# Performance work log

Measured on AMD Instinct MI355X. Metric: run time of the kernel, lower is better.

Reference implementation:

```python
import jax, jax.numpy as jnp
import numpy as np

B, T, TQ, E = 32, 200, 50, 64
P, C = 128, 64
BN_EPS = 1e-6
DICE_EPS = 1e-6


def _bn(x, g, b, m, v):
    # inference-mode batch norm over last axis
    return (x - m) * jax.lax.rsqrt(v + BN_EPS) * g + b


def _dice(x, alpha, m, v):
    # Dice activation: p = sigmoid(BN(x, no scale/shift)); out = p*x + alpha*(1-p)*x
    p = jax.nn.sigmoid((x - m) * jax.lax.rsqrt(v + DICE_EPS))
    return p * x + alpha * (1.0 - p) * x


def setup_inputs() -> dict:
    key = jax.random.key(0)
    ks = jax.random.split(key, 16)
    def g(k, shape, scale=0.05):
        return jax.random.normal(k, shape, dtype=jnp.float32) * scale
    inp = {
        "user_behavior": jax.random.normal(ks[0], (B, T, E), dtype=jnp.float32),
        "items": jax.random.normal(ks[1], (B, TQ, E), dtype=jnp.float32),
        "user_profile": jax.random.normal(ks[2], (B, P), dtype=jnp.float32),
        "context": jax.random.normal(ks[3], (B, C), dtype=jnp.float32),
        # attention MLP
        "W1": g(ks[4], (4 * E, 36)), "b1": jnp.zeros((36,), jnp.float32),
        "dice_alpha": jnp.zeros((36,), jnp.float32),
        "dice_mean": jnp.zeros((36,), jnp.float32),
        "dice_var": jnp.ones((36,), jnp.float32),
        "W2": g(ks[5], (36, 1)), "b2": jnp.zeros((1,), jnp.float32),
        # trunk MLP (input dim E+P+C = 256)
        "bn1_g": jnp.ones((E + P + C,), jnp.float32), "bn1_b": jnp.zeros((E + P + C,), jnp.float32),
        "bn1_m": jnp.zeros((E + P + C,), jnp.float32), "bn1_v": jnp.ones((E + P + C,), jnp.float32),
        "Wm1": g(ks[6], (E + P + C, 256)), "bm1": jnp.zeros((256,), jnp.float32),
        "bn2_g": jnp.ones((256,), jnp.float32), "bn2_b": jnp.zeros((256,), jnp.float32),
        "bn2_m": jnp.zeros((256,), jnp.float32), "bn2_v": jnp.ones((256,), jnp.float32),
        "Wm2": g(ks[7], (256, 128)), "bm2": jnp.zeros((128,), jnp.float32),
        "bn3_g": jnp.ones((128,), jnp.float32), "bn3_b": jnp.zeros((128,), jnp.float32),
        "bn3_m": jnp.zeros((128,), jnp.float32), "bn3_v": jnp.ones((128,), jnp.float32),
        "Wm3": g(ks[8], (128, 64)), "bm3": jnp.zeros((64,), jnp.float32),
    }
    return inp


def reference(user_behavior, items, user_profile, context,
              W1, b1, dice_alpha, dice_mean, dice_var, W2, b2,
              bn1_g, bn1_b, bn1_m, bn1_v, Wm1, bm1,
              bn2_g, bn2_b, bn2_m, bn2_v, Wm2, bm2,
              bn3_g, bn3_b, bn3_m, bn3_v, Wm3, bm3):
    b, t, e = user_behavior.shape
    tq = items.shape[1]
    # tile/concat cross product: (B, T', T, 4E)
    q = jnp.broadcast_to(user_behavior[:, None, :, :], (b, tq, t, e))
    k = jnp.broadcast_to(items[:, :, None, :], (b, tq, t, e))
    x = jnp.concatenate([q, k, q - k, q * k], axis=-1)
    x = jnp.einsum('btsf,fu->btsu', x, W1) + b1
    x = _dice(x, dice_alpha, dice_mean, dice_var)
    weight = (jnp.einsum('btsu,uo->btso', x, W2) + b2)[..., 0]  # (B, T', T)
    # weighted sum over history: (B, T', E)
    interest = jnp.einsum('bts,bse->bte', weight, user_behavior)
    # trunk MLP (dropout is identity at inference)
    up = jnp.broadcast_to(user_profile[:, None, :], (b, tq, user_profile.shape[-1]))
    cx = jnp.broadcast_to(context[:, None, :], (b, tq, context.shape[-1]))
    h = jnp.concatenate([interest, up, cx], axis=-1)
    h = _bn(h, bn1_g, bn1_b, bn1_m, bn1_v)
    h = jax.nn.relu(h @ Wm1 + bm1)
    h = _bn(h, bn2_g, bn2_b, bn2_m, bn2_v)
    h = jax.nn.relu(h @ Wm2 + bm2)
    h = _bn(h, bn3_g, bn3_b, bn3_m, bn3_v)
    h = jax.nn.relu(h @ Wm3 + bm3)
    return h
```

## Files before the change

kernel.cpp:

```cpp
#include <hip/hip_runtime.h>
#include <hip/hip_bf16.h>
#include <math.h>

#define NB  32
#define NT  200
#define NTQ 50
#define NE  64
#define NP  128
#define NC  64
#define NU  36
#define NROW (NB * NTQ)

typedef __attribute__((ext_vector_type(8))) short bf8;
typedef __attribute__((ext_vector_type(4))) float f4;

#define KW_F32   0
#define BF_BASE  57600
#define W1F_OFF  0
#define WM1F_OFF 6144
#define WM2F_OFF 71680
#define WM3F_OFF 104448
#define HH_OFF   112640

__device__ __forceinline__ short f2bf(float x) {
    __hip_bfloat16 h = __float2bfloat16(x);
    return __builtin_bit_cast(short, h);
}

__device__ __forceinline__ void pack_frag(int j, const float* W, int N, int ksc, short* dst) {
    int i    = j & 7;
    int lane = (j >> 3) & 63;
    int tile = j >> 9;
    int ks = tile % ksc;
    int nt = tile / ksc;
    int k = ks * 32 + 8 * (lane >> 4) + i;
    int n = nt * 16 + (lane & 15);
    dst[j] = f2bf(W[k * N + n]);
}

__global__ __launch_bounds__(256) void prep(
    const float* __restrict__ it,
    const float* __restrict__ W1, const float* __restrict__ b1,
    const float* __restrict__ Wm1, const float* __restrict__ Wm2, const float* __restrict__ Wm3,
    float* __restrict__ kW,
    short* __restrict__ w1f, short* __restrict__ wm1f,
    short* __restrict__ wm2f, short* __restrict__ wm3f)
{
    int idx = blockIdx.x * 256 + threadIdx.x;
    if (idx < NB * NTQ * NU) {
        int u = idx % NU, row = idx / NU;
        const float* k = it + row * NE;
        float acc = b1[u];
        #pragma unroll 4
        for (int e = 0; e < NE; ++e)
            acc = fmaf(k[e], W1[(64 + e) * NU + u] - W1[(128 + e) * NU + u], acc);
        kW[idx] = acc;
        return;
    }
    idx -= NB * NTQ * NU;
    if (idx < 6144) {
        int i = idx & 7, lane = (idx >> 3) & 63, tile = idx >> 9;
        int ks = tile & 3, nt = tile >> 2;
        int kk = ks * 32 + 8 * (lane >> 4) + i;
        int n  = nt * 16 + (lane & 15);
        float v = 0.f;
        if (n < NU) {
            v = W1[(128 + kk) * NU + n];
            if (kk < 64) v += W1[kk * NU + n];
        }
        w1f[idx] = f2bf(v);
        return;
    }
    idx -= 6144;
    if (idx < 65536) { pack_frag(idx, Wm1, 256, 8, wm1f); return; }
    idx -= 65536;
    if (idx < 32768) { pack_frag(idx, Wm2, 128, 8, wm2f); return; }
    idx -= 32768;
    if (idx < 8192)  { pack_frag(idx, Wm3,  64, 4, wm3f); return; }
}

struct AParams {
    const float *ub, *it, *kW, *W2, *b2, *da, *dm, *dv;
    const float *bn1_g, *bn1_b, *bn1_m, *bn1_v;
    const short *w1f;
    short* Hh;
};

__global__ __launch_bounds__(256) void attn(AParams P) {
    __shared__ float w_s[NT];
    __shared__ float red_s[256];

    const int tid = threadIdx.x;
    const int l = tid & 63, w = tid >> 6;
    const int tq = blockIdx.x, b = blockIdx.y;

    bf8 bfr[3][4];
    {
        const bf8* wf = (const bf8*)P.w1f;
        #pragma unroll
        for (int nt = 0; nt < 3; ++nt)
            #pragma unroll
            for (int ks = 0; ks < 4; ++ks)
                bfr[nt][ks] = wf[(nt * 4 + ks) * 64 + l];
    }

    float itv[2][8];
    {
        const float* itr = P.it + ((size_t)b * NTQ + tq) * NE;
        #pragma unroll
        for (int ks = 0; ks < 2; ++ks) {
            int e0 = ks * 32 + 8 * (l >> 4);
            f4 v0 = *(const f4*)(itr + e0);
            f4 v1 = *(const f4*)(itr + e0 + 4);
            #pragma unroll
            for (int i = 0; i < 4; ++i) { itv[ks][i] = v0[i]; itv[ks][4 + i] = v1[i]; }
        }
    }

    const int ul = l & 15;
    float kwv[3], dmv[3], drs[3], dav[3], w2v[3];
    {
        const float* kwr = P.kW + ((size_t)b * NTQ + tq) * NU;
        #pragma unroll
        for (int nt = 0; nt < 3; ++nt) {
            int u = nt * 16 + ul;
            bool v = (u < NU);
            int uc = v ? u : (NU - 1);
            kwv[nt] = v ? kwr[uc] : 0.f;
            dmv[nt] = P.dm[uc];
            drs[nt] = rsqrtf(P.dv[uc] + 1e-6f);
            dav[nt] = P.da[uc];
            w2v[nt] = v ? P.W2[uc] : 0.f;
        }
    }
    const float b2s = P.b2[0];

    for (int tt = w; tt < 13; tt += 4) {
        const int t0 = tt * 16;
        const int tA = t0 + (l & 15);

        bf8 aq[2], ap[2];
        if (tA < NT) {
            const float* ubr = P.ub + ((size_t)b * NT + tA) * NE;
            #pragma unroll
            for (int ks = 0; ks < 2; ++ks) {
                int e0 = ks * 32 + 8 * (l >> 4);
                f4 u0 = *(const f4*)(ubr + e0);
                f4 u1 = *(const f4*)(ubr + e0 + 4);
                #pragma unroll
                for (int i = 0; i < 4; ++i) {
                    aq[ks][i]     = f2bf(u0[i]);
                    aq[ks][4 + i] = f2bf(u1[i]);
                    ap[ks][i]     = f2bf(u0[i] * itv[ks][i]);
                    ap[ks][4 + i] = f2bf(u1[i] * itv[ks][4 + i]);
                }
            }
        } else {
            #pragma unroll
            for (int ks = 0; ks < 2; ++ks)
                #pragma unroll
                for (int i = 0; i < 8; ++i) { aq[ks][i] = 0; ap[ks][i] = 0; }
        }

        f4 acc[3];
        #pragma unroll
        for (int nt = 0; nt < 3; ++nt) { acc[nt][0]=0.f; acc[nt][1]=0.f; acc[nt][2]=0.f; acc[nt][3]=0.f; }
        #pragma unroll
        for (int nt = 0; nt < 3; ++nt) {
            acc[nt] = __builtin_amdgcn_mfma_f32_16x16x32_bf16(aq[0], bfr[nt][0], acc[nt], 0, 0, 0);
            acc[nt] = __builtin_amdgcn_mfma_f32_16x16x32_bf16(aq[1], bfr[nt][1], acc[nt], 0, 0, 0);
            acc[nt] = __builtin_amdgcn_mfma_f32_16x16x32_bf16(ap[0], bfr[nt][2], acc[nt], 0, 0, 0);
            acc[nt] = __builtin_amdgcn_mfma_f32_16x16x32_bf16(ap[1], bfr[nt][3], acc[nt], 0, 0, 0);
        }

        const int tD = t0 + 4 * (l >> 4);
        #pragma unroll
        for (int i = 0; i < 4; ++i) {
            int t = tD + i;
            bool tv = (t < NT);
            float val = 0.f;
            #pragma unroll
            for (int nt = 0; nt < 3; ++nt) {
                float x = acc[nt][i] + kwv[nt];
                float z = (x - dmv[nt]) * drs[nt];
                float p = 1.f / (1.f + __expf(-z));
                val += x * (dav[nt] + p * (1.f - dav[nt])) * w2v[nt];
            }
            val += __shfl_xor(val, 1);
            val += __shfl_xor(val, 2);
            val += __shfl_xor(val, 4);
            val += __shfl_xor(val, 8);
            if (ul == 0 && tv) w_s[t] = val + b2s;
        }
    }
    __syncthreads();

    {
        const int e = tid & 63, g = tid >> 6;
        const float* ubb = P.ub + (size_t)b * NT * NE;
        float s = 0.f;
        #pragma unroll 5
        for (int t = g * 50; t < g * 50 + 50; ++t)
            s = fmaf(w_s[t], ubb[t * NE + e], s);
        red_s[tid] = s;
    }
    __syncthreads();
    if (tid < 64) {
        float tot = red_s[tid] + red_s[64 + tid] + red_s[128 + tid] + red_s[192 + tid];
        float hn = (tot - P.bn1_m[tid]) * rsqrtf(P.bn1_v[tid] + 1e-6f) * P.bn1_g[tid] + P.bn1_b[tid];
        P.Hh[((size_t)b * NTQ + tq) * 64 + tid] = f2bf(hn);
    }
}

struct TParams {
    const short *Hh, *wm1f, *wm2f, *wm3f;
    const float *up, *cx;
    const float *bn1_g, *bn1_b, *bn1_m, *bn1_v;
    const float *bm1, *bm2, *bm3;
    const float *bn2_g, *bn2_b, *bn2_m, *bn2_v;
    const float *bn3_g, *bn3_b, *bn3_m, *bn3_v;
    float* out;
};

#define LSTR 264

__global__ __launch_bounds__(256) void trunk(TParams P) {
    __shared__ short Ha[16 * LSTR];
    __shared__ short Hb[16 * LSTR];

    const int tid = threadIdx.x;
    const int l = tid & 63, w = tid >> 6;
    const int row0 = blockIdx.x * 16;

    {
        const bf8* src = (const bf8*)(P.Hh + (size_t)row0 * 64);
        for (int ch = tid; ch < 16 * 8; ch += 256) {
            int r = ch >> 3, c8 = ch & 7;
            *(bf8*)&Ha[r * LSTR + c8 * 8] = src[r * 8 + c8];
        }
    }
    for (int ch = tid; ch < 16 * 192; ch += 256) {
        int r = ch / 192, c = ch % 192;
        int col = 64 + c;
        int b = (row0 + r) / NTQ;
        float val = (c < NP) ? P.up[b * NP + c] : P.cx[b * NC + (c - NP)];
        float hn = (val - P.bn1_m[col]) * rsqrtf(P.bn1_v[col] + 1e-6f)
                   * P.bn1_g[col] + P.bn1_b[col];
        Ha[r * LSTR + col] = f2bf(hn);
    }
    __syncthreads();

    const int ar = l & 15;
    const int rl = 4 * (l >> 4);
    const int nl = l & 15;

    {
        bf8 a[8];
        #pragma unroll
        for (int ks = 0; ks < 8; ++ks)
            a[ks] = *(const bf8*)&Ha[ar * LSTR + ks * 32 + 8 * (l >> 4)];
        const bf8* wf = (const bf8*)P.wm1f;
        #pragma unroll
        for (int nt0 = 0; nt0 < 4; ++nt0) {
            int nt = w * 4 + nt0;
            f4 acc; acc[0]=0.f; acc[1]=0.f; acc[2]=0.f; acc[3]=0.f;
            #pragma unroll
            for (int ks = 0; ks < 8; ++ks)
                acc = __builtin_amdgcn_mfma_f32_16x16x32_bf16(a[ks], wf[(nt * 8 + ks) * 64 + l], acc, 0, 0, 0);
            int n = nt * 16 + nl;
            float g1 = P.bn2_g[n] * rsqrtf(P.bn2_v[n] + 1e-6f);
            float c1 = P.bn2_b[n] - P.bn2_m[n] * g1;
            float bias = P.bm1[n];
            #pragma unroll
            for (int i = 0; i < 4; ++i) {
                float v = fmaxf(acc[i] + bias, 0.f);
                Hb[(rl + i) * LSTR + n] = f2bf(v * g1 + c1);
            }
        }
    }
    __syncthreads();

    {
        bf8 a[8];
        #pragma unroll
        for (int ks = 0; ks < 8; ++ks)
            a[ks] = *(const bf8*)&Hb[ar * LSTR + ks * 32 + 8 * (l >> 4)];
        const bf8* wf = (const bf8*)P.wm2f;
        #pragma unroll
        for (int nt0 = 0; nt0 < 2; ++nt0) {
            int nt = w * 2 + nt0;
            f4 acc; acc[0]=0.f; acc[1]=0.f; acc[2]=0.f; acc[3]=0.f;
            #pragma unroll
            for (int ks = 0; ks < 8; ++ks)
                acc = __builtin_amdgcn_mfma_f32_16x16x32_bf16(a[ks], wf[(nt * 8 + ks) * 64 + l], acc, 0, 0, 0);
            int n = nt * 16 + nl;
            float g1 = P.bn3_g[n] * rsqrtf(P.bn3_v[n] + 1e-6f);
            float c1 = P.bn3_b[n] - P.bn3_m[n] * g1;
            float bias = P.bm2[n];
            #pragma unroll
            for (int i = 0; i < 4; ++i) {
                float v = fmaxf(acc[i] + bias, 0.f);
                Ha[(rl + i) * LSTR + n] = f2bf(v * g1 + c1);
            }
        }
    }
    __syncthreads();

    {
        bf8 a[4];
        #pragma unroll
        for (int ks = 0; ks < 4; ++ks)
            a[ks] = *(const bf8*)&Ha[ar * LSTR + ks * 32 + 8 * (l >> 4)];
        const bf8* wf = (const bf8*)P.wm3f;
        {
            int nt = w;
            f4 acc; acc[0]=0.f; acc[1]=0.f; acc[2]=0.f; acc[3]=0.f;
            #pragma unroll
            for (int ks = 0; ks < 4; ++ks)
                acc = __builtin_amdgcn_mfma_f32_16x16x32_bf16(a[ks], wf[(nt * 4 + ks) * 64 + l], acc, 0, 0, 0);
            int n = nt * 16 + nl;
            float bias = P.bm3[n];
            #pragma unroll
            for (int i = 0; i < 4; ++i)
                P.out[(size_t)(row0 + rl + i) * 64 + n] = fmaxf(acc[i] + bias, 0.f);
        }
    }
}

extern "C" void kernel_launch(void* const* d_in, const int* in_sizes, int n_in,
                              void* d_out, int out_size, void* d_ws, size_t ws_size,
                              hipStream_t stream) {
    (void)in_sizes; (void)n_in; (void)out_size; (void)ws_size;

    const float* ub         = (const float*)d_in[0];
    const float* it         = (const float*)d_in[1];
    const float* up         = (const float*)d_in[2];
    const float* cx         = (const float*)d_in[3];
    const float* W1         = (const float*)d_in[4];
    const float* b1         = (const float*)d_in[5];
    const float* dice_alpha = (const float*)d_in[6];
    const float* dice_mean  = (const float*)d_in[7];
    const float* dice_var   = (const float*)d_in[8];
    const float* W2         = (const float*)d_in[9];
    const float* b2         = (const float*)d_in[10];
    const float* bn1_g      = (const float*)d_in[11];
    const float* bn1_b      = (const float*)d_in[12];
    const float* bn1_m      = (const float*)d_in[13];
    const float* bn1_v      = (const float*)d_in[14];
    const float* Wm1        = (const float*)d_in[15];
    const float* bm1        = (const float*)d_in[16];
    const float* bn2_g      = (const float*)d_in[17];
    const float* bn2_b      = (const float*)d_in[18];
    const float* bn2_m      = (const float*)d_in[19];
    const float* bn2_v      = (const float*)d_in[20];
    const float* Wm2        = (const float*)d_in[21];
    const float* bm2        = (const float*)d_in[22];
    const float* bn3_g      = (const float*)d_in[23];
    const float* bn3_b      = (const float*)d_in[24];
    const float* bn3_m      = (const float*)d_in[25];
    const float* bn3_v      = (const float*)d_in[26];
    const float* Wm3        = (const float*)d_in[27];
    const float* bm3        = (const float*)d_in[28];

    float* kW  = (float*)d_ws + KW_F32;
    short* wsb = (short*)((float*)d_ws + BF_BASE);
    short* w1f  = wsb + W1F_OFF;
    short* wm1f = wsb + WM1F_OFF;
    short* wm2f = wsb + WM2F_OFF;
    short* wm3f = wsb + WM3F_OFF;
    short* Hh   = wsb + HH_OFF;

    const int prep_total = NB * NTQ * NU + 6144 + 65536 + 32768 + 8192;
    prep<<<(prep_total + 255) / 256, 256, 0, stream>>>(
        it, W1, b1, Wm1, Wm2, Wm3,
        kW, w1f, wm1f, wm2f, wm3f);

    AParams A;
    A.ub = ub; A.it = it; A.kW = kW;
    A.W2 = W2; A.b2 = b2; A.da = dice_alpha; A.dm = dice_mean; A.dv = dice_var;
    A.bn1_g = bn1_g; A.bn1_b = bn1_b; A.bn1_m = bn1_m; A.bn1_v = bn1_v;
    A.w1f = w1f; A.Hh = Hh;
    attn<<<dim3(NTQ, NB), 256, 0, stream>>>(A);

    TParams T;
    T.Hh = Hh; T.wm1f = wm1f; T.wm2f = wm2f; T.wm3f = wm3f;
    T.up = up; T.cx = cx;
    T.bn1_g = bn1_g; T.bn1_b = bn1_b; T.bn1_m = bn1_m; T.bn1_v = bn1_v;
    T.bm1 = bm1; T.bm2 = bm2; T.bm3 = bm3;
    T.bn2_g = bn2_g; T.bn2_b = bn2_b; T.bn2_m = bn2_m; T.bn2_v = bn2_v;
    T.bn3_g = bn3_g; T.bn3_b = bn3_b; T.bn3_m = bn3_m; T.bn3_v = bn3_v;
    T.out = (float*)d_out;
    trunk<<<NROW / 16, 256, 0, stream>>>(T);
}
```

Measured before the change: 153.1 us.

## Fold prep kernel into attention kernel and compute item projection via MFMA

Removes the separate prep launch. Each attention block now builds its W1 bf16 fragments straight from fp32 W1, and extra blocks appended to the attention grid pack the trunk weights. The per-item term kW is no longer precomputed in fp32. It is computed inside each block with two extra MFMAs on the bf16 item vector, and the result seeds the accumulator. This saves a launch and a round trip through workspace memory, at the cost of redundant per-block weight conversion (18 bf8 fragments built from scattered global loads) and bf16 precision for the item term.

```diff
diff --git a/kernel.cpp b/kernel.cpp
--- a/kernel.cpp
+++ b/kernel.cpp
@@ -14,13 +14,14 @@
 typedef __attribute__((ext_vector_type(8))) short bf8;
 typedef __attribute__((ext_vector_type(4))) float f4;
 
-#define KW_F32   0
-#define BF_BASE  57600
-#define W1F_OFF  0
-#define WM1F_OFF 6144
-#define WM2F_OFF 71680
-#define WM3F_OFF 104448
-#define HH_OFF   112640
+#define WM1F_OFF 0
+#define WM2F_OFF 65536
+#define WM3F_OFF 98304
+#define HH_OFF   106496
+
+#define ATTN_BLOCKS 1600
+#define PACK_ELEMS  (65536 + 32768 + 8192)
+#define PACK_BLOCKS ((PACK_ELEMS + 255) / 256)
 
 __device__ __forceinline__ short f2bf(float x) {
     __hip_bfloat16 h = __float2bfloat16(x);
@@ -38,73 +39,61 @@
     dst[j] = f2bf(W[k * N + n]);
 }
 
-__global__ __launch_bounds__(256) void prep(
-    const float* __restrict__ it,
-    const float* __restrict__ W1, const float* __restrict__ b1,
-    const float* __restrict__ Wm1, const float* __restrict__ Wm2, const float* __restrict__ Wm3,
-    float* __restrict__ kW,
-    short* __restrict__ w1f, short* __restrict__ wm1f,
-    short* __restrict__ wm2f, short* __restrict__ wm3f)
-{
-    int idx = blockIdx.x * 256 + threadIdx.x;
-    if (idx < NB * NTQ * NU) {
-        int u = idx % NU, row = idx / NU;
-        const float* k = it + row * NE;
-        float acc = b1[u];
-        #pragma unroll 4
-        for (int e = 0; e < NE; ++e)
-            acc = fmaf(k[e], W1[(64 + e) * NU + u] - W1[(128 + e) * NU + u], acc);
-        kW[idx] = acc;
-        return;
-    }
-    idx -= NB * NTQ * NU;
-    if (idx < 6144) {
-        int i = idx & 7, lane = (idx >> 3) & 63, tile = idx >> 9;
-        int ks = tile & 3, nt = tile >> 2;
-        int kk = ks * 32 + 8 * (lane >> 4) + i;
-        int n  = nt * 16 + (lane & 15);
-        float v = 0.f;
-        if (n < NU) {
-            v = W1[(128 + kk) * NU + n];
-            if (kk < 64) v += W1[kk * NU + n];
-        }
-        w1f[idx] = f2bf(v);
-        return;
-    }
-    idx -= 6144;
-    if (idx < 65536) { pack_frag(idx, Wm1, 256, 8, wm1f); return; }
-    idx -= 65536;
-    if (idx < 32768) { pack_frag(idx, Wm2, 128, 8, wm2f); return; }
-    idx -= 32768;
-    if (idx < 8192)  { pack_frag(idx, Wm3,  64, 4, wm3f); return; }
-}
-
 struct AParams {
-    const float *ub, *it, *kW, *W2, *b2, *da, *dm, *dv;
+    const float *ub, *it, *W1, *b1, *W2, *b2, *da, *dm, *dv;
     const float *bn1_g, *bn1_b, *bn1_m, *bn1_v;
-    const short *w1f;
+    const float *Wm1, *Wm2, *Wm3;
+    short *wm1f, *wm2f, *wm3f;
     short* Hh;
 };
 
 __global__ __launch_bounds__(256) void attn(AParams P) {
+    const int bid = blockIdx.x;
+    const int tid = threadIdx.x;
+
+    if (bid >= ATTN_BLOCKS) {
+        int j = (bid - ATTN_BLOCKS) * 256 + tid;
+        if (j < 65536) { pack_frag(j, P.Wm1, 256, 8, P.wm1f); return; }
+        j -= 65536;
+        if (j < 32768) { pack_frag(j, P.Wm2, 128, 8, P.wm2f); return; }
+        j -= 32768;
+        if (j < 8192)  { pack_frag(j, P.Wm3,  64, 4, P.wm3f); }
+        return;
+    }
+
     __shared__ float w_s[NT];
     __shared__ float red_s[256];
 
-    const int tid = threadIdx.x;
     const int l = tid & 63, w = tid >> 6;
-    const int tq = blockIdx.x, b = blockIdx.y;
-
-    bf8 bfr[3][4];
-    {
-        const bf8* wf = (const bf8*)P.w1f;
-        #pragma unroll
-        for (int nt = 0; nt < 3; ++nt)
-            #pragma unroll
-            for (int ks = 0; ks < 4; ++ks)
-                bfr[nt][ks] = wf[(nt * 4 + ks) * 64 + l];
+    const int tq = bid % NTQ, b = bid / NTQ;
+
+    const int ul = l & 15;
+    bf8 bfr[3][6];
+    #pragma unroll
+    for (int nt = 0; nt < 3; ++nt) {
+        int n = nt * 16 + ul;
+        bool nv = (n < NU);
+        #pragma unroll
+        for (int ks = 0; ks < 6; ++ks) {
+            #pragma unroll
+            for (int i = 0; i < 8; ++i) {
+                int kk = ks * 32 + 8 * (l >> 4) + i;
+                float v = 0.f;
+                if (nv) {
+                    if (kk < 128) {
+                        v = P.W1[(128 + kk) * NU + n];
+                        if (kk < 64) v += P.W1[kk * NU + n];
+                    } else {
+                        v = P.W1[(kk - 64) * NU + n] - P.W1[kk * NU + n];
+                    }
+                }
+                bfr[nt][ks][i] = f2bf(v);
+            }
+        }
     }
 
     float itv[2][8];
+    bf8 ak[2];
     {
         const float* itr = P.it + ((size_t)b * NTQ + tq) * NE;
         #pragma unroll
@@ -113,25 +102,33 @@
             f4 v0 = *(const f4*)(itr + e0);
             f4 v1 = *(const f4*)(itr + e0 + 4);
             #pragma unroll
-            for (int i = 0; i < 4; ++i) { itv[ks][i] = v0[i]; itv[ks][4 + i] = v1[i]; }
-        }
-    }
-
-    const int ul = l & 15;
-    float kwv[3], dmv[3], drs[3], dav[3], w2v[3];
-    {
-        const float* kwr = P.kW + ((size_t)b * NTQ + tq) * NU;
-        #pragma unroll
-        for (int nt = 0; nt < 3; ++nt) {
-            int u = nt * 16 + ul;
-            bool v = (u < NU);
-            int uc = v ? u : (NU - 1);
-            kwv[nt] = v ? kwr[uc] : 0.f;
-            dmv[nt] = P.dm[uc];
-            drs[nt] = rsqrtf(P.dv[uc] + 1e-6f);
-            dav[nt] = P.da[uc];
-            w2v[nt] = v ? P.W2[uc] : 0.f;
-        }
+            for (int i = 0; i < 4; ++i) {
+                itv[ks][i] = v0[i]; itv[ks][4 + i] = v1[i];
+                ak[ks][i] = f2bf(v0[i]); ak[ks][4 + i] = f2bf(v1[i]);
+            }
+        }
+    }
+
+    f4 acc0[3];
+    #pragma unroll
+    for (int nt = 0; nt < 3; ++nt) {
+        f4 z; z[0]=0.f; z[1]=0.f; z[2]=0.f; z[3]=0.f;
+        z = __builtin_amdgcn_mfma_f32_16x16x32_bf16(ak[0], bfr[nt][4], z, 0, 0, 0);
+        z = __builtin_amdgcn_mfma_f32_16x16x32_bf16(ak[1], bfr[nt][5], z, 0, 0, 0);
+        acc0[nt] = z;
+    }
+
+    float b1v[3], dmv[3], drs[3], dav[3], w2v[3];
+    #pragma unroll
+    for (int nt = 0; nt < 3; ++nt) {
+        int u = nt * 16 + ul;
+        bool v = (u < NU);
+        int uc = v ? u : (NU - 1);
+        b1v[nt] = P.b1[uc];
+        dmv[nt] = P.dm[uc];
+        drs[nt] = rsqrtf(P.dv[uc] + 1e-6f);
+        dav[nt] = P.da[uc];
+        w2v[nt] = v ? P.W2[uc] : 0.f;
     }
     const float b2s = P.b2[0];
 
@@ -164,7 +161,7 @@
 
         f4 acc[3];
         #pragma unroll
-        for (int nt = 0; nt < 3; ++nt) { acc[nt][0]=0.f; acc[nt][1]=0.f; acc[nt][2]=0.f; acc[nt][3]=0.f; }
+        for (int nt = 0; nt < 3; ++nt) acc[nt] = acc0[nt];
         #pragma unroll
         for (int nt = 0; nt < 3; ++nt) {
             acc[nt] = __builtin_amdgcn_mfma_f32_16x16x32_bf16(aq[0], bfr[nt][0], acc[nt], 0, 0, 0);
@@ -181,7 +178,7 @@
             float val = 0.f;
             #pragma unroll
             for (int nt = 0; nt < 3; ++nt) {
-                float x = acc[nt][i] + kwv[nt];
+                float x = acc[nt][i] + b1v[nt];
                 float z = (x - dmv[nt]) * drs[nt];
                 float p = 1.f / (1.f + __expf(-z));
                 val += x * (dav[nt] + p * (1.f - dav[nt])) * w2v[nt];
@@ -362,25 +359,20 @@
     const float* Wm3        = (const float*)d_in[27];
     const float* bm3        = (const float*)d_in[28];
 
-    float* kW  = (float*)d_ws + KW_F32;
-    short* wsb = (short*)((float*)d_ws + BF_BASE);
-    short* w1f  = wsb + W1F_OFF;
+    short* wsb  = (short*)d_ws;
     short* wm1f = wsb + WM1F_OFF;
     short* wm2f = wsb + WM2F_OFF;
     short* wm3f = wsb + WM3F_OFF;
     short* Hh   = wsb + HH_OFF;
 
-    const int prep_total = NB * NTQ * NU + 6144 + 65536 + 32768 + 8192;
-    prep<<<(prep_total + 255) / 256, 256, 0, stream>>>(
-        it, W1, b1, Wm1, Wm2, Wm3,
-        kW, w1f, wm1f, wm2f, wm3f);
-
     AParams A;
-    A.ub = ub; A.it = it; A.kW = kW;
+    A.ub = ub; A.it = it; A.W1 = W1; A.b1 = b1;
     A.W2 = W2; A.b2 = b2; A.da = dice_alpha; A.dm = dice_mean; A.dv = dice_var;
     A.bn1_g = bn1_g; A.bn1_b = bn1_b; A.bn1_m = bn1_m; A.bn1_v = bn1_v;
-    A.w1f = w1f; A.Hh = Hh;
-    attn<<<dim3(NTQ, NB), 256, 0, stream>>>(A);
+    A.Wm1 = Wm1; A.Wm2 = Wm2; A.Wm3 = Wm3;
+    A.wm1f = wm1f; A.wm2f = wm2f; A.wm3f = wm3f;
+    A.Hh = Hh;
+    attn<<<ATTN_BLOCKS + PACK_BLOCKS, 256, 0, stream>>>(A);
 
     TParams T;
     T.Hh = Hh; T.wm1f = wm1f; T.wm2f = wm2f; T.wm3f = wm3f;
```

Result: slower. 224.2 us (+46.5%).
